# Kernel optimization log

Measured on AMD Instinct MI355X. Metric: run time of the kernel, lower is better.

Reference implementation:

```python
import jax, jax.numpy as jnp
import numpy as np

B, S, D, H = 2, 2048, 1024, 16
DEPTH = D // H


def setup_inputs() -> dict:
    key = jax.random.key(0)
    ks = jax.random.split(key, 10)
    std = 1.0 / np.sqrt(D)
    v = jax.random.normal(ks[0], (B, S, D), jnp.float32)
    q = jax.random.normal(ks[1], (B, S, D), jnp.float32)
    k = jax.random.normal(ks[2], (B, S, D), jnp.float32)
    # padding mask: 1.0 at masked (padded) key positions, 0.0 elsewhere
    mask = (jax.random.uniform(ks[3], (B, 1, 1, S)) < 0.1).astype(jnp.float32)
    Wq = jax.random.normal(ks[4], (D, D), jnp.float32) * std
    bq = jnp.zeros((D,), jnp.float32)
    Wv = jax.random.normal(ks[5], (D, D), jnp.float32) * std
    bv = jnp.zeros((D,), jnp.float32)
    Wo = jax.random.normal(ks[6], (D, D), jnp.float32) * std
    bo = jnp.zeros((D,), jnp.float32)
    return {"v": v, "q": q, "k": k, "mask": mask,
            "Wq": Wq, "bq": bq, "Wv": Wv, "bv": bv, "Wo": Wo, "bo": bo}


def _split_heads(x):
    # (B, S, D) -> (B, H, S, depth)
    return x.reshape(B, S, H, DEPTH).transpose(0, 2, 1, 3)


def reference(v, q, k, mask, Wq, bq, Wv, bv, Wo, bo):
    # NOTE: faithful to source, keys are projected with the QUERY weights
    # (mixedK = self.wQuery(k) in the original code).
    Q = _split_heads(q @ Wq + bq)
    K = _split_heads(k @ Wq + bq)
    V = _split_heads(v @ Wv + bv)
    scale = 1.0 / jnp.sqrt(jnp.asarray(DEPTH, jnp.float32))
    logits = jnp.einsum('bhqd,bhkd->bhqk', Q, K) * scale
    logits = logits + mask * (-1e9)
    attn = jax.nn.softmax(logits, axis=-1)
    out = jnp.einsum('bhqk,bhkd->bhqd', attn, V)
    out = out.transpose(0, 2, 1, 3).reshape(B, S, D)
    return out @ Wo + bo
```

## Files before the change

### kernel.cpp

```cpp
#include <hip/hip_runtime.h>
#include <cstddef>


namespace {

constexpr int Ss = 2048;
constexpr int Dd = 1024;
constexpr int Mm = 4096;
constexpr int NT = Ss / 64;
constexpr float QSCALE = 0.18033688f;

typedef unsigned short u16;
typedef __attribute__((ext_vector_type(8))) __bf16 bf16x8;
typedef __attribute__((ext_vector_type(4))) float f32x4;
typedef __attribute__((ext_vector_type(16))) float f32x16;
typedef __attribute__((ext_vector_type(4))) unsigned int u32x4;
typedef __attribute__((ext_vector_type(2))) unsigned int u32x2;
typedef __attribute__((ext_vector_type(8))) unsigned short us8;

__device__ __forceinline__ u16 bfc(float f) {
  __bf16 h = (__bf16)f;
  return __builtin_bit_cast(u16, h);
}
__device__ __forceinline__ unsigned pack2(float lo, float hi) {
  return (unsigned)bfc(lo) | ((unsigned)bfc(hi) << 16);
}

__device__ __forceinline__ void gload_lds16(const void* g, void* l) {
  __builtin_amdgcn_global_load_lds(
      (__attribute__((address_space(1))) void*)g,
      (__attribute__((address_space(3))) void*)l, 16, 0, 0);
}

__device__ __forceinline__ f32x4 mfma16(bf16x8 a, bf16x8 b, f32x4 c) {
  return __builtin_amdgcn_mfma_f32_16x16x32_bf16(a, b, c, 0, 0, 0);
}
__device__ __forceinline__ f32x16 mfma32(bf16x8 a, bf16x8 b, f32x16 c) {
  return __builtin_amdgcn_mfma_f32_32x32x16_bf16(a, b, c, 0, 0, 0);
}
__device__ __forceinline__ float exp2_fast(float x) {
  return __builtin_amdgcn_exp2f(x);
}

__device__ __forceinline__ void pl32swap(unsigned& a, unsigned& b) {
#if __has_builtin(__builtin_amdgcn_permlane32_swap)
  u32x2 r = __builtin_amdgcn_permlane32_swap(a, b, false, false);
  a = r[0];
  b = r[1];
#else
  unsigned ax = (unsigned)__shfl_xor((int)a, 32);
  unsigned bx = (unsigned)__shfl_xor((int)b, 32);
  bool hi = (threadIdx.x & 63) >= 32;
  unsigned na = hi ? bx : a;
  unsigned nb = hi ? b : ax;
  a = na;
  b = nb;
#endif
}

#define PIPE_BARRIER_V(N)                                  \
  do {                                                     \
    asm volatile("s_waitcnt vmcnt(" #N ")" ::: "memory");  \
    __builtin_amdgcn_sched_barrier(0);                     \
    __builtin_amdgcn_s_barrier();                          \
    __builtin_amdgcn_sched_barrier(0);                     \
  } while (0)

__device__ __forceinline__ int swz(int row, int col) {
  return row * 64 + ((((col >> 3) ^ (row & 7)) << 3) | (col & 7));
}
__device__ __forceinline__ int src_col(int lane) {
  return ((lane & 7) ^ (lane >> 3)) * 8;
}

__global__ __launch_bounds__(256) void wt_transpose(const float* __restrict__ W0,
                                                    const float* __restrict__ W1,
                                                    const float* __restrict__ W2,
                                                    u16* __restrict__ wsbase) {
  const float* W = (blockIdx.z == 0) ? W0 : (blockIdx.z == 1) ? W1 : W2;
  u16* WT = wsbase + (size_t)blockIdx.z * (1024 * 1024);
  __shared__ float tile[32][33];
  const int tid = threadIdx.x;
  const int tx = tid & 31;
  const int ty = tid >> 5;
  const int n0 = blockIdx.x * 32;
  const int k0 = blockIdx.y * 32;
#pragma unroll
  for (int i = 0; i < 4; ++i)
    tile[ty + i * 8][tx] = W[(size_t)(k0 + ty + i * 8) * 1024 + n0 + tx];
  __syncthreads();
  const int r = tid >> 3;
  const int c4 = (tid & 7) * 4;
  ushort4 o4 = make_ushort4(bfc(tile[c4 + 0][r]), bfc(tile[c4 + 1][r]),
                            bfc(tile[c4 + 2][r]), bfc(tile[c4 + 3][r]));
  *(ushort4*)(&WT[(size_t)(n0 + r) * 1024 + k0 + c4]) = o4;
}

__global__ __launch_bounds__(256) void cvt_bf16(const float* __restrict__ q,
                                                const float* __restrict__ k,
                                                const float* __restrict__ v,
                                                u16* __restrict__ qb,
                                                u16* __restrict__ kb,
                                                u16* __restrict__ vb) {
  const int which = (int)(blockIdx.x >> 11);
  const int blk = (int)(blockIdx.x & 2047);
  const float* src = (which == 0) ? q : (which == 1) ? k : v;
  u16* dst = (which == 0) ? qb : (which == 1) ? kb : vb;
  const int base = (blk * 256 + (int)threadIdx.x) * 8;
  const float4 a = *(const float4*)(src + base);
  const float4 b = *(const float4*)(src + base + 4);
  us8 o;
  o[0] = bfc(a.x); o[1] = bfc(a.y); o[2] = bfc(a.z); o[3] = bfc(a.w);
  o[4] = bfc(b.x); o[5] = bfc(b.y); o[6] = bfc(b.z); o[7] = bfc(b.w);
  *(us8*)(dst + base) = o;
}

__global__ __launch_bounds__(256) void proj_qkv(
    const u16* __restrict__ qb, const u16* __restrict__ kb,
    const u16* __restrict__ vb, const u16* __restrict__ WqT,
    const u16* __restrict__ WvT, const float* __restrict__ bq,
    const float* __restrict__ bv, const float* __restrict__ maskf,
    u16* __restrict__ Qp, u16* __restrict__ Kp, u16* __restrict__ VpT) {
  constexpr int K = 1024, N = 1024, M = 4096;
  __shared__ u16 As[128 * 64];
  __shared__ u16 Bs[128 * 64];
  const int lin = (int)blockIdx.x;
  const int xcd = lin & 7;
  const int j = lin >> 3;
  const int panel = xcd * 12 + (j >> 3);
  const int ntile = j & 7;
  const int z = panel >> 5;
  const int mtile = panel & 31;
  const int n0 = ntile * 128;
  const int m0 = mtile * 128;

  const u16* A = (z == 0) ? qb : (z == 1) ? kb : vb;
  const u16* Bt = (z == 2) ? WvT : WqT;
  const float* bias = (z == 2) ? bv : bq;
  const float cscale = (z == 0) ? QSCALE : 1.0f;

  const int tid = threadIdx.x;
  const int wid = tid >> 6;
  const int lane = tid & 63;
  const int g = lane >> 4;
  const int lr = lane & 15;
  const int wr = wid >> 1, wc = wid & 1;

  const f32x4 zero = {0.f, 0.f, 0.f, 0.f};
  f32x4 acc[4][4];
#pragma unroll
  for (int m = 0; m < 4; ++m)
#pragma unroll
    for (int n = 0; n < 4; ++n) acc[m][n] = zero;

  for (int kt = 0; kt < 16; ++kt) {
#pragma unroll
    for (int jj = 0; jj < 4; ++jj) {
      int rb = (wid * 4 + jj) * 8;
      gload_lds16(&A[(size_t)(m0 + rb + (lane >> 3)) * K + kt * 64 + src_col(lane)],
                  &As[rb * 64]);
      gload_lds16(&Bt[(size_t)(n0 + rb + (lane >> 3)) * K + kt * 64 + src_col(lane)],
                  &Bs[rb * 64]);
    }
    __syncthreads();
#pragma unroll
    for (int kk = 0; kk < 2; ++kk) {
      bf16x8 a[4], b[4];
#pragma unroll
      for (int m = 0; m < 4; ++m)
        a[m] = *(const bf16x8*)(&As[swz(wr * 64 + m * 16 + lr, kk * 32 + g * 8)]);
#pragma unroll
      for (int n = 0; n < 4; ++n)
        b[n] = *(const bf16x8*)(&Bs[swz(wc * 64 + n * 16 + lr, kk * 32 + g * 8)]);
#pragma unroll
      for (int m = 0; m < 4; ++m)
#pragma unroll
        for (int n = 0; n < 4; ++n) acc[m][n] = mfma16(a[m], b[n], acc[m][n]);
    }
    __syncthreads();
  }

#pragma unroll
  for (int n = 0; n < 4; ++n) {
    const int col = n0 + wc * 64 + n * 16 + lr;
    const float bv_ = bias[col];
#pragma unroll
    for (int m = 0; m < 4; ++m) {
      const int rowb = m0 + wr * 64 + m * 16 + g * 4;
      if (z == 2) {
        const f32x4 mk = *(const f32x4*)(&maskf[rowb]);
        ushort4 o4;
        o4.x = (mk[0] != 0.f) ? (u16)0 : bfc(acc[m][n][0] + bv_);
        o4.y = (mk[1] != 0.f) ? (u16)0 : bfc(acc[m][n][1] + bv_);
        o4.z = (mk[2] != 0.f) ? (u16)0 : bfc(acc[m][n][2] + bv_);
        o4.w = (mk[3] != 0.f) ? (u16)0 : bfc(acc[m][n][3] + bv_);
        *(ushort4*)(&VpT[(size_t)col * M + rowb]) = o4;
      } else {
        u16* Cp = (z == 0) ? Qp : Kp;
#pragma unroll
        for (int r = 0; r < 4; ++r)
          Cp[(size_t)(rowb + r) * N + col] = bfc((acc[m][n][r] + bv_) * cscale);
      }
    }
  }
}

__global__ __launch_bounds__(256) void gemm_o(const u16* __restrict__ Ap,
                                              const u16* __restrict__ Bt,
                                              const float* __restrict__ bias,
                                              float* __restrict__ Cp) {
  constexpr int K = 1024, N = 1024;
  __shared__ u16 As[3][128 * 64];
  __shared__ u16 Bs[3][64 * 64];
  const int lin = (int)blockIdx.x;
  const int xcd = lin & 7;
  const int j = lin >> 3;
  const int mtile = xcd * 4 + (j >> 4);
  const int ntile = j & 15;
  const int n0 = ntile * 64;
  const int m0 = mtile * 128;

  const int tid = threadIdx.x;
  const int wid = tid >> 6;
  const int lane = tid & 63;
  const int g = lane >> 4;
  const int lr = lane & 15;

  const f32x4 zero = {0.f, 0.f, 0.f, 0.f};
  f32x4 acc[2][4];
#pragma unroll
  for (int m = 0; m < 2; ++m)
#pragma unroll
    for (int n = 0; n < 4; ++n) acc[m][n] = zero;

  auto stage = [&](int kt, u16* as, u16* bs) {
#pragma unroll
    for (int jj = 0; jj < 4; ++jj) {
      int rb = (wid * 4 + jj) * 8;
      gload_lds16(&Ap[(size_t)(m0 + rb + (lane >> 3)) * K + kt * 64 + src_col(lane)],
                  as + rb * 64);
    }
#pragma unroll
    for (int jj = 0; jj < 2; ++jj) {
      int rb = (wid * 2 + jj) * 8;
      gload_lds16(&Bt[(size_t)(n0 + rb + (lane >> 3)) * K + kt * 64 + src_col(lane)],
                  bs + rb * 64);
    }
  };

  stage(0, As[0], Bs[0]);
  stage(1, As[1], Bs[1]);

  int b0 = 0;
  for (int kt = 0; kt < 16; ++kt) {
    if (kt < 15) PIPE_BARRIER_V(6);
    else         PIPE_BARRIER_V(0);
    if (kt + 2 < 16) {
      int b2 = b0 + 2; if (b2 >= 3) b2 -= 3;
      stage(kt + 2, As[b2], Bs[b2]);
    }
    const u16* as = As[b0];
    const u16* bs = Bs[b0];
#pragma unroll
    for (int kk = 0; kk < 2; ++kk) {
      bf16x8 a[2], b[4];
#pragma unroll
      for (int m = 0; m < 2; ++m)
        a[m] = *(const bf16x8*)(&as[swz(wid * 32 + m * 16 + lr, kk * 32 + g * 8)]);
#pragma unroll
      for (int n = 0; n < 4; ++n)
        b[n] = *(const bf16x8*)(&bs[swz(n * 16 + lr, kk * 32 + g * 8)]);
#pragma unroll
      for (int m = 0; m < 2; ++m)
#pragma unroll
        for (int n = 0; n < 4; ++n) acc[m][n] = mfma16(a[m], b[n], acc[m][n]);
    }
    b0 = (b0 == 2) ? 0 : b0 + 1;
  }
#pragma unroll
  for (int n = 0; n < 4; ++n) {
    const int col = n0 + n * 16 + lr;
    const float bv_ = bias[col];
#pragma unroll
    for (int m = 0; m < 2; ++m) {
      const int rowb = m0 + wid * 32 + m * 16 + g * 4;
#pragma unroll
      for (int r = 0; r < 4; ++r)
        Cp[(size_t)(rowb + r) * N + col] = acc[m][n][r] + bv_;
    }
  }
}

__global__ __launch_bounds__(512) void attn32(const u16* __restrict__ Qp,
                                              const u16* __restrict__ Kp,
                                              const u16* __restrict__ VpT,
                                              const float* __restrict__ mask,
                                              u16* __restrict__ Op) {
  __shared__ u16 smem[6 * 64 * 64];
  __shared__ u16 validall[Ss];
  const int tid = threadIdx.x;
  const int wid = tid >> 6;
  const int lane = tid & 63;
  const int l31 = lane & 31;
  const int hi = lane >> 5;
  const int qq = wid & 3;
  const int kh = wid >> 2;
  const int lin = (int)(blockIdx.x + (blockIdx.y << 4));
  const int wl = (lin & 7) * 64 + (lin >> 3);
  const int qt = wl & 15;
  const int bh = wl >> 4;
  const int b = bh >> 4;
  const int h = bh & 15;
  const int q0 = qt * 128;
  const size_t base = ((size_t)b * Ss) * Dd + (size_t)h * 64;
  const size_t vbase = (size_t)h * 64 * Mm + (size_t)b * Ss;
  const int qrow = q0 + qq * 32 + l31;

  auto stageKV = [&](int t, int buf) {
    const int key0 = t * 64;
    const int rb = wid * 8;
    gload_lds16(&Kp[base + (size_t)(key0 + rb + (lane >> 3)) * Dd + src_col(lane)],
                smem + buf * 4096 + rb * 64);
    gload_lds16(&VpT[vbase + (size_t)(rb + (lane >> 3)) * Mm + key0 + src_col(lane)],
                smem + (3 + buf) * 4096 + rb * 64);
  };

  float4 mk0, mk1;
  if (tid < 256) {
    mk0 = *(const float4*)(&mask[(size_t)b * Ss + tid * 8]);
    mk1 = *(const float4*)(&mask[(size_t)b * Ss + tid * 8 + 4]);
  }
  bf16x8 qf[4];
#pragma unroll
  for (int ks = 0; ks < 4; ++ks)
    qf[ks] = *(const bf16x8*)(&Qp[base + (size_t)qrow * Dd + ks * 16 + hi * 8]);

  stageKV(0, 0);
  stageKV(1, 1);

  if (tid < 256) {
    us8 vv;
    vv[0] = (mk0.x != 0.f) ? (u16)0 : (u16)0x3F80;
    vv[1] = (mk0.y != 0.f) ? (u16)0 : (u16)0x3F80;
    vv[2] = (mk0.z != 0.f) ? (u16)0 : (u16)0x3F80;
    vv[3] = (mk0.w != 0.f) ? (u16)0 : (u16)0x3F80;
    vv[4] = (mk1.x != 0.f) ? (u16)0 : (u16)0x3F80;
    vv[5] = (mk1.y != 0.f) ? (u16)0 : (u16)0x3F80;
    vv[6] = (mk1.z != 0.f) ? (u16)0 : (u16)0x3F80;
    vv[7] = (mk1.w != 0.f) ? (u16)0 : (u16)0x3F80;
    *(us8*)(&validall[tid * 8]) = vv;
  }
  asm volatile("s_waitcnt lgkmcnt(0)" ::: "memory");
  __builtin_amdgcn_sched_barrier(0);
  __builtin_amdgcn_s_barrier();
  __builtin_amdgcn_sched_barrier(0);

  f32x16 oacc[2], lacc, zero16;
#pragma unroll
  for (int r = 0; r < 16; ++r) zero16[r] = 0.f;
#pragma unroll
  for (int i = 0; i < 2; ++i)
#pragma unroll
    for (int r = 0; r < 16; ++r) oacc[i][r] = 0.f;
#pragma unroll
  for (int r = 0; r < 16; ++r) lacc[r] = 0.f;

  int b0 = 0;
  for (int t = 0; t < NT; ++t) {
    if (t < NT - 1) PIPE_BARRIER_V(2);
    else            PIPE_BARRIER_V(0);
    if (t + 2 < NT) {
      int b2 = b0 + 2; if (b2 >= 3) b2 -= 3;
      stageKV(t + 2, b2);
    }
    const u16* ks = smem + b0 * 4096;
    const u16* vt = smem + (3 + b0) * 4096;

    f32x16 sacc;
    {
      bf16x8 kf = *(const bf16x8*)(&ks[swz(kh * 32 + l31, 0 * 16 + hi * 8)]);
      sacc = mfma32(kf, qf[0], zero16);
    }
    __builtin_amdgcn_s_setprio(1);
#pragma unroll
    for (int ks_ = 1; ks_ < 4; ++ks_) {
      bf16x8 kf = *(const bf16x8*)(&ks[swz(kh * 32 + l31, ks_ * 16 + hi * 8)]);
      sacc = mfma32(kf, qf[ks_], sacc);
    }
    __builtin_amdgcn_s_setprio(0);

#pragma unroll
    for (int r = 0; r < 16; ++r) sacc[r] = exp2_fast(sacc[r]);

    bf16x8 pa[2];
#pragma unroll
    for (int slot = 0; slot < 2; ++slot) {
      const int bse = slot * 8;
      unsigned A0 = pack2(sacc[bse + 0], sacc[bse + 1]);
      unsigned A1 = pack2(sacc[bse + 2], sacc[bse + 3]);
      unsigned B0 = pack2(sacc[bse + 4], sacc[bse + 5]);
      unsigned B1 = pack2(sacc[bse + 6], sacc[bse + 7]);
      pl32swap(A0, B0);
      pl32swap(A1, B1);
      u32x4 w = {A0, A1, B0, B1};
      pa[slot] = __builtin_bit_cast(bf16x8, w);
    }

    __builtin_amdgcn_s_setprio(1);
#pragma unroll
    for (int slot = 0; slot < 2; ++slot) {
      const int kbase = t * 64 + kh * 32 + slot * 16 + hi * 8;
      bf16x8 vd = *(const bf16x8*)(&validall[kbase]);
#pragma unroll
      for (int dsub = 0; dsub < 2; ++dsub) {
        bf16x8 vf = *(const bf16x8*)(
            &vt[swz(dsub * 32 + l31, kh * 32 + slot * 16 + hi * 8)]);
        oacc[dsub] = mfma32(pa[slot], vf, oacc[dsub]);
      }
      lacc = mfma32(pa[slot], vd, lacc);
    }
    __builtin_amdgcn_s_setprio(0);

    b0 = (b0 == 2) ? 0 : b0 + 1;
  }

  __syncthreads();
  float* rbuf = (float*)smem;
  if (kh == 1) {
    float* p = rbuf + qq * 3072 + lane;
#pragma unroll
    for (int r = 0; r < 16; ++r) p[r * 64] = oacc[0][r];
#pragma unroll
    for (int r = 0; r < 16; ++r) p[(16 + r) * 64] = oacc[1][r];
#pragma unroll
    for (int r = 0; r < 16; ++r) p[(32 + r) * 64] = lacc[r];
  }
  __syncthreads();
  if (kh == 0) {
    const float* p = rbuf + qq * 3072 + lane;
#pragma unroll
    for (int r = 0; r < 16; ++r) oacc[0][r] += p[r * 64];
#pragma unroll
    for (int r = 0; r < 16; ++r) oacc[1][r] += p[(16 + r) * 64];
#pragma unroll
    for (int r = 0; r < 16; ++r) lacc[r] += p[(32 + r) * 64];

    float rl[16];
#pragma unroll
    for (int r = 0; r < 16; ++r) rl[r] = __builtin_amdgcn_rcpf(lacc[r]);
#pragma unroll
    for (int dsub = 0; dsub < 2; ++dsub) {
      const int col = h * 64 + dsub * 32 + l31;
#pragma unroll
      for (int r = 0; r < 16; ++r) {
        const int row = q0 + qq * 32 + (r & 3) + 8 * (r >> 2) + 4 * hi;
        Op[((size_t)b * Ss + row) * Dd + col] = bfc(oacc[dsub][r] * rl[r]);
      }
    }
  }
}

}

extern "C" void kernel_launch(void* const* d_in, const int* in_sizes, int n_in,
                              void* d_out, int out_size, void* d_ws, size_t ws_size,
                              hipStream_t stream) {
  (void)in_sizes; (void)n_in; (void)out_size; (void)ws_size;
  const float* v = (const float*)d_in[0];
  const float* q = (const float*)d_in[1];
  const float* k = (const float*)d_in[2];
  const float* mask = (const float*)d_in[3];
  const float* Wq = (const float*)d_in[4];
  const float* bq = (const float*)d_in[5];
  const float* Wv = (const float*)d_in[6];
  const float* bv = (const float*)d_in[7];
  const float* Wo = (const float*)d_in[8];
  const float* bo = (const float*)d_in[9];
  float* out = (float*)d_out;

  constexpr size_t MEG = 1024 * 1024;
  u16* ws = (u16*)d_ws;
  u16* WqT = ws;
  u16* WvT = ws + 1 * MEG;
  u16* WoT = ws + 2 * MEG;
  u16* qb  = ws + 3 * MEG;
  u16* kb  = ws + 7 * MEG;
  u16* vb  = ws + 11 * MEG;
  u16* Qp  = ws + 15 * MEG;
  u16* Kp  = ws + 19 * MEG;
  u16* VpT = ws + 23 * MEG;
  u16* AO  = qb;

  wt_transpose<<<dim3(32, 32, 3), 256, 0, stream>>>(Wq, Wv, Wo, ws);
  cvt_bf16<<<dim3(6144), 256, 0, stream>>>(q, k, v, qb, kb, vb);
  proj_qkv<<<dim3(768), 256, 0, stream>>>(qb, kb, vb, WqT, WvT, bq, bv, mask,
                                          Qp, Kp, VpT);
  attn32<<<dim3(16, 32), 512, 0, stream>>>(Qp, Kp, VpT, mask, AO);
  gemm_o<<<dim3(512), 256, 0, stream>>>(AO, WoT, bo, out);
}
```

Before: 130.0 us.

## Split attention over two key halves and merge partials in a combine kernel

The attention kernel now splits the 2048 keys into two halves handled by separate blocks, which doubles the grid. Each block writes unnormalized bf16 partial outputs and fp32 row sums to workspace, and a new combine kernel adds the two halves and normalizes. The K/V staging also drops from triple to double buffering, which shrinks LDS so more blocks can be resident per CU. In exchange it adds a kernel launch, extra global traffic for the partials, a shallower load pipeline, and rounding of the partial outputs to bf16 before they are summed.

```diff
diff --git a/kernel.cpp b/kernel.cpp
--- a/kernel.cpp
+++ b/kernel.cpp
@@ -7,7 +7,6 @@
 constexpr int Ss = 2048;
 constexpr int Dd = 1024;
 constexpr int Mm = 4096;
-constexpr int NT = Ss / 64;
 constexpr float QSCALE = 0.18033688f;
 
 typedef unsigned short u16;
@@ -21,6 +20,9 @@
 __device__ __forceinline__ u16 bfc(float f) {
   __bf16 h = (__bf16)f;
   return __builtin_bit_cast(u16, h);
+}
+__device__ __forceinline__ float bf2f(u16 u) {
+  return __builtin_bit_cast(float, (unsigned)u << 16);
 }
 __device__ __forceinline__ unsigned pack2(float lo, float hi) {
   return (unsigned)bfc(lo) | ((unsigned)bfc(hi) << 16);
@@ -295,9 +297,10 @@
                                               const u16* __restrict__ Kp,
                                               const u16* __restrict__ VpT,
                                               const float* __restrict__ mask,
-                                              u16* __restrict__ Op) {
-  __shared__ u16 smem[6 * 64 * 64];
-  __shared__ u16 validall[Ss];
+                                              u16* __restrict__ Opart,
+                                              float* __restrict__ lpart) {
+  __shared__ u16 smem[4 * 64 * 64];
+  __shared__ u16 valid[1024];
   const int tid = threadIdx.x;
   const int wid = tid >> 6;
   const int lane = tid & 63;
@@ -305,40 +308,42 @@
   const int hi = lane >> 5;
   const int qq = wid & 3;
   const int kh = wid >> 2;
-  const int lin = (int)(blockIdx.x + (blockIdx.y << 4));
-  const int wl = (lin & 7) * 64 + (lin >> 3);
+  const int lin = (int)(blockIdx.x + (blockIdx.y << 5));
+  const int wl = (lin & 7) * 128 + (lin >> 3);
   const int qt = wl & 15;
-  const int bh = wl >> 4;
+  const int bhks = wl >> 4;
+  const int ks = bhks & 1;
+  const int bh = bhks >> 1;
   const int b = bh >> 4;
   const int h = bh & 15;
   const int q0 = qt * 128;
   const size_t base = ((size_t)b * Ss) * Dd + (size_t)h * 64;
   const size_t vbase = (size_t)h * 64 * Mm + (size_t)b * Ss;
   const int qrow = q0 + qq * 32 + l31;
+  const int pidx = (bh * 16 + qt) * 2 + ks;
 
   auto stageKV = [&](int t, int buf) {
-    const int key0 = t * 64;
+    const int key0 = ks * 1024 + t * 64;
     const int rb = wid * 8;
     gload_lds16(&Kp[base + (size_t)(key0 + rb + (lane >> 3)) * Dd + src_col(lane)],
                 smem + buf * 4096 + rb * 64);
     gload_lds16(&VpT[vbase + (size_t)(rb + (lane >> 3)) * Mm + key0 + src_col(lane)],
-                smem + (3 + buf) * 4096 + rb * 64);
+                smem + (2 + buf) * 4096 + rb * 64);
   };
 
   float4 mk0, mk1;
-  if (tid < 256) {
-    mk0 = *(const float4*)(&mask[(size_t)b * Ss + tid * 8]);
-    mk1 = *(const float4*)(&mask[(size_t)b * Ss + tid * 8 + 4]);
+  if (tid < 128) {
+    mk0 = *(const float4*)(&mask[(size_t)b * Ss + ks * 1024 + tid * 8]);
+    mk1 = *(const float4*)(&mask[(size_t)b * Ss + ks * 1024 + tid * 8 + 4]);
   }
   bf16x8 qf[4];
 #pragma unroll
-  for (int ks = 0; ks < 4; ++ks)
-    qf[ks] = *(const bf16x8*)(&Qp[base + (size_t)qrow * Dd + ks * 16 + hi * 8]);
+  for (int d = 0; d < 4; ++d)
+    qf[d] = *(const bf16x8*)(&Qp[base + (size_t)qrow * Dd + d * 16 + hi * 8]);
 
   stageKV(0, 0);
-  stageKV(1, 1);
-
-  if (tid < 256) {
+
+  if (tid < 128) {
     us8 vv;
     vv[0] = (mk0.x != 0.f) ? (u16)0 : (u16)0x3F80;
     vv[1] = (mk0.y != 0.f) ? (u16)0 : (u16)0x3F80;
@@ -348,7 +353,7 @@
     vv[5] = (mk1.y != 0.f) ? (u16)0 : (u16)0x3F80;
     vv[6] = (mk1.z != 0.f) ? (u16)0 : (u16)0x3F80;
     vv[7] = (mk1.w != 0.f) ? (u16)0 : (u16)0x3F80;
-    *(us8*)(&validall[tid * 8]) = vv;
+    *(us8*)(&valid[tid * 8]) = vv;
   }
   asm volatile("s_waitcnt lgkmcnt(0)" ::: "memory");
   __builtin_amdgcn_sched_barrier(0);
@@ -365,27 +370,22 @@
 #pragma unroll
   for (int r = 0; r < 16; ++r) lacc[r] = 0.f;
 
-  int b0 = 0;
-  for (int t = 0; t < NT; ++t) {
-    if (t < NT - 1) PIPE_BARRIER_V(2);
-    else            PIPE_BARRIER_V(0);
-    if (t + 2 < NT) {
-      int b2 = b0 + 2; if (b2 >= 3) b2 -= 3;
-      stageKV(t + 2, b2);
-    }
-    const u16* ks = smem + b0 * 4096;
-    const u16* vt = smem + (3 + b0) * 4096;
+  for (int t = 0; t < 16; ++t) {
+    PIPE_BARRIER_V(0);
+    if (t + 1 < 16) stageKV(t + 1, (t + 1) & 1);
+    const u16* ksb = smem + (t & 1) * 4096;
+    const u16* vtb = smem + (2 + (t & 1)) * 4096;
 
     f32x16 sacc;
     {
-      bf16x8 kf = *(const bf16x8*)(&ks[swz(kh * 32 + l31, 0 * 16 + hi * 8)]);
+      bf16x8 kf = *(const bf16x8*)(&ksb[swz(kh * 32 + l31, 0 * 16 + hi * 8)]);
       sacc = mfma32(kf, qf[0], zero16);
     }
     __builtin_amdgcn_s_setprio(1);
 #pragma unroll
-    for (int ks_ = 1; ks_ < 4; ++ks_) {
-      bf16x8 kf = *(const bf16x8*)(&ks[swz(kh * 32 + l31, ks_ * 16 + hi * 8)]);
-      sacc = mfma32(kf, qf[ks_], sacc);
+    for (int d = 1; d < 4; ++d) {
+      bf16x8 kf = *(const bf16x8*)(&ksb[swz(kh * 32 + l31, d * 16 + hi * 8)]);
+      sacc = mfma32(kf, qf[d], sacc);
     }
     __builtin_amdgcn_s_setprio(0);
 
@@ -410,54 +410,81 @@
 #pragma unroll
     for (int slot = 0; slot < 2; ++slot) {
       const int kbase = t * 64 + kh * 32 + slot * 16 + hi * 8;
-      bf16x8 vd = *(const bf16x8*)(&validall[kbase]);
+      bf16x8 vd = *(const bf16x8*)(&valid[kbase]);
 #pragma unroll
       for (int dsub = 0; dsub < 2; ++dsub) {
         bf16x8 vf = *(const bf16x8*)(
-            &vt[swz(dsub * 32 + l31, kh * 32 + slot * 16 + hi * 8)]);
+            &vtb[swz(dsub * 32 + l31, kh * 32 + slot * 16 + hi * 8)]);
         oacc[dsub] = mfma32(pa[slot], vf, oacc[dsub]);
       }
       lacc = mfma32(pa[slot], vd, lacc);
     }
     __builtin_amdgcn_s_setprio(0);
-
-    b0 = (b0 == 2) ? 0 : b0 + 1;
-  }
-
-  __syncthreads();
+  }
+
   float* rbuf = (float*)smem;
-  if (kh == 1) {
-    float* p = rbuf + qq * 3072 + lane;
-#pragma unroll
-    for (int r = 0; r < 16; ++r) p[r * 64] = oacc[0][r];
-#pragma unroll
-    for (int r = 0; r < 16; ++r) p[(16 + r) * 64] = oacc[1][r];
-#pragma unroll
-    for (int r = 0; r < 16; ++r) p[(32 + r) * 64] = lacc[r];
-  }
-  __syncthreads();
-  if (kh == 0) {
-    const float* p = rbuf + qq * 3072 + lane;
-#pragma unroll
-    for (int r = 0; r < 16; ++r) oacc[0][r] += p[r * 64];
-#pragma unroll
-    for (int r = 0; r < 16; ++r) oacc[1][r] += p[(16 + r) * 64];
-#pragma unroll
-    for (int r = 0; r < 16; ++r) lacc[r] += p[(32 + r) * 64];
-
-    float rl[16];
-#pragma unroll
-    for (int r = 0; r < 16; ++r) rl[r] = __builtin_amdgcn_rcpf(lacc[r]);
-#pragma unroll
-    for (int dsub = 0; dsub < 2; ++dsub) {
-      const int col = h * 64 + dsub * 32 + l31;
-#pragma unroll
-      for (int r = 0; r < 16; ++r) {
-        const int row = q0 + qq * 32 + (r & 3) + 8 * (r >> 2) + 4 * hi;
-        Op[((size_t)b * Ss + row) * Dd + col] = bfc(oacc[dsub][r] * rl[r]);
+  for (int round = 0; round < 2; ++round) {
+    __syncthreads();
+    if ((qq >> 1) == round && kh == 1) {
+      float* p = rbuf + (qq & 1) * 3072 + lane;
+#pragma unroll
+      for (int r = 0; r < 16; ++r) p[r * 64] = oacc[0][r];
+#pragma unroll
+      for (int r = 0; r < 16; ++r) p[(16 + r) * 64] = oacc[1][r];
+#pragma unroll
+      for (int r = 0; r < 16; ++r) p[(32 + r) * 64] = lacc[r];
+    }
+    __syncthreads();
+    if ((qq >> 1) == round && kh == 0) {
+      const float* p = rbuf + (qq & 1) * 3072 + lane;
+#pragma unroll
+      for (int r = 0; r < 16; ++r) oacc[0][r] += p[r * 64];
+#pragma unroll
+      for (int r = 0; r < 16; ++r) oacc[1][r] += p[(16 + r) * 64];
+#pragma unroll
+      for (int r = 0; r < 16; ++r) lacc[r] += p[(32 + r) * 64];
+
+      u16* ob = Opart + (size_t)pidx * 8192;
+#pragma unroll
+      for (int dsub = 0; dsub < 2; ++dsub)
+#pragma unroll
+        for (int r = 0; r < 16; ++r) {
+          const int rl = qq * 32 + (r & 3) + 8 * (r >> 2) + 4 * hi;
+          ob[rl * 64 + dsub * 32 + l31] = bfc(oacc[dsub][r]);
+        }
+      if (l31 == 0) {
+#pragma unroll
+        for (int r = 0; r < 16; ++r) {
+          const int rl = qq * 32 + (r & 3) + 8 * (r >> 2) + 4 * hi;
+          lpart[(size_t)pidx * 128 + rl] = lacc[r];
+        }
       }
     }
   }
+}
+
+__global__ __launch_bounds__(256) void combine(const u16* __restrict__ Opart,
+                                               const float* __restrict__ lpart,
+                                               u16* __restrict__ AO) {
+  const int e = (int)blockIdx.x * 256 + (int)threadIdx.x;
+  const int d8 = e & 7;
+  const int h = (e >> 3) & 15;
+  const int row = e >> 7;
+  const int b = row >> 11;
+  const int srow = row & 2047;
+  const int qt = srow >> 7;
+  const int r = srow & 127;
+  const int pbase = ((b * 16 + h) * 16 + qt) * 2;
+  const size_t off = (size_t)r * 64 + d8 * 8;
+
+  const us8 o0 = *(const us8*)(&Opart[(size_t)pbase * 8192 + off]);
+  const us8 o1 = *(const us8*)(&Opart[(size_t)(pbase + 1) * 8192 + off]);
+  const float l = lpart[(size_t)pbase * 128 + r] + lpart[(size_t)(pbase + 1) * 128 + r];
+  const float rl = __builtin_amdgcn_rcpf(l);
+  us8 o;
+#pragma unroll
+  for (int j = 0; j < 8; ++j) o[j] = bfc((bf2f(o0[j]) + bf2f(o1[j])) * rl);
+  *(us8*)(&AO[(size_t)row * 1024 + h * 64 + d8 * 8]) = o;
 }
 
 }
@@ -490,11 +517,14 @@
   u16* Kp  = ws + 19 * MEG;
   u16* VpT = ws + 23 * MEG;
   u16* AO  = qb;
+  u16* Opart = kb;
+  float* lpart = (float*)WqT;
 
   wt_transpose<<<dim3(32, 32, 3), 256, 0, stream>>>(Wq, Wv, Wo, ws);
   cvt_bf16<<<dim3(6144), 256, 0, stream>>>(q, k, v, qb, kb, vb);
   proj_qkv<<<dim3(768), 256, 0, stream>>>(qb, kb, vb, WqT, WvT, bq, bv, mask,
                                           Qp, Kp, VpT);
-  attn32<<<dim3(16, 32), 512, 0, stream>>>(Qp, Kp, VpT, mask, AO);
+  attn32<<<dim3(32, 32), 512, 0, stream>>>(Qp, Kp, VpT, mask, Opart, lpart);
+  combine<<<dim3(2048), 256, 0, stream>>>(Opart, lpart, AO);
   gemm_o<<<dim3(512), 256, 0, stream>>>(AO, WoT, bo, out);
 }
```

Measured after the change: 138.8 us. +6.8%, slower.

## Restructure attention tiles to 128 keys with 2x4 wave split and additive mask

Applied to the files above, without the earlier changes.

The attention kernel now stages 128-key K/V tiles with double buffering instead of 64-key triple buffering. The eight waves are split as 2 query groups by 4 key groups, and each wave handles 64 query rows so every K fragment load feeds two MFMA chains. The padding mask becomes an additive bias preloaded into the score accumulator, and the row sums are computed with shuffles rather than an extra MFMA against a validity vector. The cost is a four-way cross-wave reduction of outputs and sums at the end, done in several synchronised passes, plus more registers per wave, which may reduce occupancy.

```diff
diff --git a/kernel.cpp b/kernel.cpp
--- a/kernel.cpp
+++ b/kernel.cpp
@@ -7,8 +7,8 @@
 constexpr int Ss = 2048;
 constexpr int Dd = 1024;
 constexpr int Mm = 4096;
-constexpr int NT = Ss / 64;
 constexpr float QSCALE = 0.18033688f;
+constexpr float NEG2 = -1.442695041e9f;
 
 typedef unsigned short u16;
 typedef __attribute__((ext_vector_type(8))) __bf16 bf16x8;
@@ -61,6 +61,13 @@
 #define PIPE_BARRIER_V(N)                                  \
   do {                                                     \
     asm volatile("s_waitcnt vmcnt(" #N ")" ::: "memory");  \
+    __builtin_amdgcn_sched_barrier(0);                     \
+    __builtin_amdgcn_s_barrier();                          \
+    __builtin_amdgcn_sched_barrier(0);                     \
+  } while (0)
+
+#define PLAIN_BARRIER()                                    \
+  do {                                                     \
     __builtin_amdgcn_sched_barrier(0);                     \
     __builtin_amdgcn_s_barrier();                          \
     __builtin_amdgcn_sched_barrier(0);                     \
@@ -296,15 +303,16 @@
                                               const u16* __restrict__ VpT,
                                               const float* __restrict__ mask,
                                               u16* __restrict__ Op) {
-  __shared__ u16 smem[6 * 64 * 64];
-  __shared__ u16 validall[Ss];
+  __shared__ u16 Ks[2][128 * 64];
+  __shared__ u16 Vt[2][2][64 * 64];
+  __shared__ float msall[2048];
   const int tid = threadIdx.x;
   const int wid = tid >> 6;
   const int lane = tid & 63;
   const int l31 = lane & 31;
   const int hi = lane >> 5;
-  const int qq = wid & 3;
-  const int kh = wid >> 2;
+  const int qq = wid & 1;
+  const int kh = wid >> 1;
   const int lin = (int)(blockIdx.x + (blockIdx.y << 4));
   const int wl = (lin & 7) * 64 + (lin >> 3);
   const int qt = wl & 15;
@@ -314,149 +322,195 @@
   const int q0 = qt * 128;
   const size_t base = ((size_t)b * Ss) * Dd + (size_t)h * 64;
   const size_t vbase = (size_t)h * 64 * Mm + (size_t)b * Ss;
-  const int qrow = q0 + qq * 32 + l31;
 
   auto stageKV = [&](int t, int buf) {
-    const int key0 = t * 64;
-    const int rb = wid * 8;
-    gload_lds16(&Kp[base + (size_t)(key0 + rb + (lane >> 3)) * Dd + src_col(lane)],
-                smem + buf * 4096 + rb * 64);
-    gload_lds16(&VpT[vbase + (size_t)(rb + (lane >> 3)) * Mm + key0 + src_col(lane)],
-                smem + (3 + buf) * 4096 + rb * 64);
+    const int key0 = t * 128;
+#pragma unroll
+    for (int j = 0; j < 2; ++j) {
+      const int rb = wid * 16 + j * 8;
+      gload_lds16(&Kp[base + (size_t)(key0 + rb + (lane >> 3)) * Dd + src_col(lane)],
+                  &Ks[buf][rb * 64]);
+    }
+#pragma unroll
+    for (int kc = 0; kc < 2; ++kc) {
+      const int rb = wid * 8;
+      gload_lds16(&VpT[vbase + (size_t)(rb + (lane >> 3)) * Mm + key0 + kc * 64 + src_col(lane)],
+                  &Vt[buf][kc][rb * 64]);
+    }
   };
 
-  float4 mk0, mk1;
-  if (tid < 256) {
-    mk0 = *(const float4*)(&mask[(size_t)b * Ss + tid * 8]);
-    mk1 = *(const float4*)(&mask[(size_t)b * Ss + tid * 8 + 4]);
-  }
-  bf16x8 qf[4];
-#pragma unroll
-  for (int ks = 0; ks < 4; ++ks)
-    qf[ks] = *(const bf16x8*)(&Qp[base + (size_t)qrow * Dd + ks * 16 + hi * 8]);
+  bf16x8 qf[2][4];
+#pragma unroll
+  for (int qs = 0; qs < 2; ++qs) {
+    const int qrow = q0 + qq * 64 + qs * 32 + l31;
+#pragma unroll
+    for (int d = 0; d < 4; ++d)
+      qf[qs][d] = *(const bf16x8*)(&Qp[base + (size_t)qrow * Dd + d * 16 + hi * 8]);
+  }
+  const float4 mk = *(const float4*)(&mask[(size_t)b * Ss + tid * 4]);
 
   stageKV(0, 0);
   stageKV(1, 1);
 
-  if (tid < 256) {
-    us8 vv;
-    vv[0] = (mk0.x != 0.f) ? (u16)0 : (u16)0x3F80;
-    vv[1] = (mk0.y != 0.f) ? (u16)0 : (u16)0x3F80;
-    vv[2] = (mk0.z != 0.f) ? (u16)0 : (u16)0x3F80;
-    vv[3] = (mk0.w != 0.f) ? (u16)0 : (u16)0x3F80;
-    vv[4] = (mk1.x != 0.f) ? (u16)0 : (u16)0x3F80;
-    vv[5] = (mk1.y != 0.f) ? (u16)0 : (u16)0x3F80;
-    vv[6] = (mk1.z != 0.f) ? (u16)0 : (u16)0x3F80;
-    vv[7] = (mk1.w != 0.f) ? (u16)0 : (u16)0x3F80;
-    *(us8*)(&validall[tid * 8]) = vv;
+  {
+    f32x4 s = {mk.x * NEG2, mk.y * NEG2, mk.z * NEG2, mk.w * NEG2};
+    *(f32x4*)(&msall[tid * 4]) = s;
   }
   asm volatile("s_waitcnt lgkmcnt(0)" ::: "memory");
-  __builtin_amdgcn_sched_barrier(0);
-  __builtin_amdgcn_s_barrier();
-  __builtin_amdgcn_sched_barrier(0);
-
-  f32x16 oacc[2], lacc, zero16;
-#pragma unroll
-  for (int r = 0; r < 16; ++r) zero16[r] = 0.f;
-#pragma unroll
-  for (int i = 0; i < 2; ++i)
-#pragma unroll
-    for (int r = 0; r < 16; ++r) oacc[i][r] = 0.f;
-#pragma unroll
-  for (int r = 0; r < 16; ++r) lacc[r] = 0.f;
-
-  int b0 = 0;
-  for (int t = 0; t < NT; ++t) {
-    if (t < NT - 1) PIPE_BARRIER_V(2);
-    else            PIPE_BARRIER_V(0);
-    if (t + 2 < NT) {
-      int b2 = b0 + 2; if (b2 >= 3) b2 -= 3;
-      stageKV(t + 2, b2);
-    }
-    const u16* ks = smem + b0 * 4096;
-    const u16* vt = smem + (3 + b0) * 4096;
-
-    f32x16 sacc;
-    {
-      bf16x8 kf = *(const bf16x8*)(&ks[swz(kh * 32 + l31, 0 * 16 + hi * 8)]);
-      sacc = mfma32(kf, qf[0], zero16);
-    }
+  PLAIN_BARRIER();
+
+  f32x16 oacc[2][2];
+#pragma unroll
+  for (int qs = 0; qs < 2; ++qs)
+#pragma unroll
+    for (int ds = 0; ds < 2; ++ds)
+#pragma unroll
+      for (int r = 0; r < 16; ++r) oacc[qs][ds][r] = 0.f;
+  float lsum[2] = {0.f, 0.f};
+
+  for (int t = 0; t < 16; ++t) {
+    if (t < 15) PIPE_BARRIER_V(4);
+    else        PIPE_BARRIER_V(0);
+    const u16* ksb = Ks[t & 1];
+    const u16* vkc = &Vt[t & 1][kh >> 1][0];
+    const int koff = (kh & 1) * 32;
+    const float* msp = &msall[t * 128 + kh * 32];
+
+    bf16x8 kf[4];
+#pragma unroll
+    for (int d = 0; d < 4; ++d)
+      kf[d] = *(const bf16x8*)(&ksb[swz(kh * 32 + l31, d * 16 + hi * 8)]);
+
+    f32x4 mm[4];
+#pragma unroll
+    for (int a = 0; a < 4; ++a)
+      mm[a] = *(const f32x4*)(&msp[a * 8 + hi * 4]);
+    f32x16 sacc[2];
+#pragma unroll
+    for (int qs = 0; qs < 2; ++qs)
+#pragma unroll
+      for (int a = 0; a < 4; ++a)
+#pragma unroll
+        for (int jj = 0; jj < 4; ++jj) sacc[qs][a * 4 + jj] = mm[a][jj];
+
     __builtin_amdgcn_s_setprio(1);
 #pragma unroll
-    for (int ks_ = 1; ks_ < 4; ++ks_) {
-      bf16x8 kf = *(const bf16x8*)(&ks[swz(kh * 32 + l31, ks_ * 16 + hi * 8)]);
-      sacc = mfma32(kf, qf[ks_], sacc);
-    }
+    for (int qs = 0; qs < 2; ++qs)
+#pragma unroll
+      for (int d = 0; d < 4; ++d)
+        sacc[qs] = mfma32(kf[d], qf[qs][d], sacc[qs]);
     __builtin_amdgcn_s_setprio(0);
 
 #pragma unroll
-    for (int r = 0; r < 16; ++r) sacc[r] = exp2_fast(sacc[r]);
-
-    bf16x8 pa[2];
-#pragma unroll
-    for (int slot = 0; slot < 2; ++slot) {
-      const int bse = slot * 8;
-      unsigned A0 = pack2(sacc[bse + 0], sacc[bse + 1]);
-      unsigned A1 = pack2(sacc[bse + 2], sacc[bse + 3]);
-      unsigned B0 = pack2(sacc[bse + 4], sacc[bse + 5]);
-      unsigned B1 = pack2(sacc[bse + 6], sacc[bse + 7]);
-      pl32swap(A0, B0);
-      pl32swap(A1, B1);
-      u32x4 w = {A0, A1, B0, B1};
-      pa[slot] = __builtin_bit_cast(bf16x8, w);
-    }
-
+    for (int qs = 0; qs < 2; ++qs)
+#pragma unroll
+      for (int r = 0; r < 16; ++r) sacc[qs][r] = exp2_fast(sacc[qs][r]);
+
+#pragma unroll
+    for (int qs = 0; qs < 2; ++qs) {
+      float sm = sacc[qs][0];
+#pragma unroll
+      for (int r = 1; r < 16; ++r) sm += sacc[qs][r];
+      lsum[qs] += sm + __shfl_xor(sm, 32);
+    }
+
+    bf16x8 pa[2][2];
+#pragma unroll
+    for (int qs = 0; qs < 2; ++qs)
+#pragma unroll
+      for (int slot = 0; slot < 2; ++slot) {
+        const int bse = slot * 8;
+        unsigned A0 = pack2(sacc[qs][bse + 0], sacc[qs][bse + 1]);
+        unsigned A1 = pack2(sacc[qs][bse + 2], sacc[qs][bse + 3]);
+        unsigned B0 = pack2(sacc[qs][bse + 4], sacc[qs][bse + 5]);
+        unsigned B1 = pack2(sacc[qs][bse + 6], sacc[qs][bse + 7]);
+        pl32swap(A0, B0);
+        pl32swap(A1, B1);
+        u32x4 w = {A0, A1, B0, B1};
+        pa[qs][slot] = __builtin_bit_cast(bf16x8, w);
+      }
+
+    bf16x8 vfr[2][2];
+#pragma unroll
+    for (int ds = 0; ds < 2; ++ds)
+#pragma unroll
+      for (int slot = 0; slot < 2; ++slot)
+        vfr[ds][slot] = *(const bf16x8*)(
+            &vkc[swz(ds * 32 + l31, koff + slot * 16 + hi * 8)]);
     __builtin_amdgcn_s_setprio(1);
 #pragma unroll
-    for (int slot = 0; slot < 2; ++slot) {
-      const int kbase = t * 64 + kh * 32 + slot * 16 + hi * 8;
-      bf16x8 vd = *(const bf16x8*)(&validall[kbase]);
-#pragma unroll
-      for (int dsub = 0; dsub < 2; ++dsub) {
-        bf16x8 vf = *(const bf16x8*)(
-            &vt[swz(dsub * 32 + l31, kh * 32 + slot * 16 + hi * 8)]);
-        oacc[dsub] = mfma32(pa[slot], vf, oacc[dsub]);
+    for (int qs = 0; qs < 2; ++qs)
+#pragma unroll
+      for (int ds = 0; ds < 2; ++ds)
+#pragma unroll
+        for (int slot = 0; slot < 2; ++slot)
+          oacc[qs][ds] = mfma32(pa[qs][slot], vfr[ds][slot], oacc[qs][ds]);
+    __builtin_amdgcn_s_setprio(0);
+
+    PLAIN_BARRIER();
+    if (t + 2 < 16) stageKV(t + 2, t & 1);
+  }
+
+  PLAIN_BARRIER();
+  if (kh > 0) {
+#pragma unroll
+    for (int qs = 0; qs < 2; ++qs)
+      msall[qs * 192 + (kh - 1) * 64 + qq * 32 + l31] = lsum[qs];
+  }
+  __syncthreads();
+  f32x4 rlv[2];
+  if (kh == 0) {
+#pragma unroll
+    for (int qs = 0; qs < 2; ++qs) {
+      float lt = lsum[qs];
+#pragma unroll
+      for (int j = 0; j < 3; ++j)
+        lt += msall[qs * 192 + j * 64 + qq * 32 + l31];
+      msall[512 + qs * 64 + qq * 32 + l31] = __builtin_amdgcn_rcpf(lt);
+    }
+    asm volatile("s_waitcnt lgkmcnt(0)" ::: "memory");
+    __builtin_amdgcn_sched_barrier(0);
+  }
+  float* rbuf = (float*)&Ks[0][0];
+#pragma unroll
+  for (int qs = 0; qs < 2; ++qs)
+#pragma unroll
+    for (int ds = 0; ds < 2; ++ds) {
+      __syncthreads();
+      if (kh > 0) {
+        float* p = rbuf + ((kh - 1) * 2 + qq) * 1024 + lane;
+#pragma unroll
+        for (int r = 0; r < 16; ++r) p[r * 64] = oacc[qs][ds][r];
       }
-      lacc = mfma32(pa[slot], vd, lacc);
-    }
-    __builtin_amdgcn_s_setprio(0);
-
-    b0 = (b0 == 2) ? 0 : b0 + 1;
-  }
-
-  __syncthreads();
-  float* rbuf = (float*)smem;
-  if (kh == 1) {
-    float* p = rbuf + qq * 3072 + lane;
-#pragma unroll
-    for (int r = 0; r < 16; ++r) p[r * 64] = oacc[0][r];
-#pragma unroll
-    for (int r = 0; r < 16; ++r) p[(16 + r) * 64] = oacc[1][r];
-#pragma unroll
-    for (int r = 0; r < 16; ++r) p[(32 + r) * 64] = lacc[r];
-  }
-  __syncthreads();
+      __syncthreads();
+      if (kh == 0) {
+#pragma unroll
+        for (int j = 0; j < 3; ++j) {
+          const float* p = rbuf + (j * 2 + qq) * 1024 + lane;
+#pragma unroll
+          for (int r = 0; r < 16; ++r) oacc[qs][ds][r] += p[r * 64];
+        }
+      }
+    }
   if (kh == 0) {
-    const float* p = rbuf + qq * 3072 + lane;
-#pragma unroll
-    for (int r = 0; r < 16; ++r) oacc[0][r] += p[r * 64];
-#pragma unroll
-    for (int r = 0; r < 16; ++r) oacc[1][r] += p[(16 + r) * 64];
-#pragma unroll
-    for (int r = 0; r < 16; ++r) lacc[r] += p[(32 + r) * 64];
-
-    float rl[16];
-#pragma unroll
-    for (int r = 0; r < 16; ++r) rl[r] = __builtin_amdgcn_rcpf(lacc[r]);
-#pragma unroll
-    for (int dsub = 0; dsub < 2; ++dsub) {
-      const int col = h * 64 + dsub * 32 + l31;
-#pragma unroll
-      for (int r = 0; r < 16; ++r) {
-        const int row = q0 + qq * 32 + (r & 3) + 8 * (r >> 2) + 4 * hi;
-        Op[((size_t)b * Ss + row) * Dd + col] = bfc(oacc[dsub][r] * rl[r]);
+    f32x4 rl[2][4];
+#pragma unroll
+    for (int qs = 0; qs < 2; ++qs)
+#pragma unroll
+      for (int a = 0; a < 4; ++a)
+        rl[qs][a] = *(const f32x4*)(&msall[512 + qs * 64 + qq * 32 + a * 8 + hi * 4]);
+#pragma unroll
+    for (int qs = 0; qs < 2; ++qs)
+#pragma unroll
+      for (int ds = 0; ds < 2; ++ds) {
+        const int col = h * 64 + ds * 32 + l31;
+#pragma unroll
+        for (int r = 0; r < 16; ++r) {
+          const int row = q0 + qq * 64 + qs * 32 + (r & 3) + 8 * (r >> 2) + 4 * hi;
+          Op[((size_t)b * Ss + row) * Dd + col] =
+              bfc(oacc[qs][ds][r] * rl[qs][r >> 2][r & 3]);
+        }
       }
-    }
   }
 }
 
```

Result: slower. 145.5 us (+11.9%).

## Merge prep kernels and restructure attention loop with additive mask and 4-buffer staging

Applied to the files above, without the earlier changes.

Fuses the weight transpose and bf16 conversion into one prep launch to remove a kernel launch. In the attention kernel, the mask is now added to the logits by seeding the QK accumulator with a scaled mask bias, replacing the extra MFMA that computed the row sum against a validity vector. The row sum is instead formed by in-register adds plus a lane shuffle. The K/V pipeline goes from a triple buffer to four buffers loaded two tiles at a time, with one barrier per pair of tiles. This uses more LDS and may expose more load latency, because each barrier waits for all outstanding loads (vmcnt 0).

```diff
diff --git a/kernel.cpp b/kernel.cpp
--- a/kernel.cpp
+++ b/kernel.cpp
@@ -7,8 +7,8 @@
 constexpr int Ss = 2048;
 constexpr int Dd = 1024;
 constexpr int Mm = 4096;
-constexpr int NT = Ss / 64;
 constexpr float QSCALE = 0.18033688f;
+constexpr float NEG2 = -1.442695041e9f;
 
 typedef unsigned short u16;
 typedef __attribute__((ext_vector_type(8))) __bf16 bf16x8;
@@ -73,46 +73,51 @@
   return ((lane & 7) ^ (lane >> 3)) * 8;
 }
 
-__global__ __launch_bounds__(256) void wt_transpose(const float* __restrict__ W0,
-                                                    const float* __restrict__ W1,
-                                                    const float* __restrict__ W2,
-                                                    u16* __restrict__ wsbase) {
-  const float* W = (blockIdx.z == 0) ? W0 : (blockIdx.z == 1) ? W1 : W2;
-  u16* WT = wsbase + (size_t)blockIdx.z * (1024 * 1024);
+__global__ __launch_bounds__(256) void prep(const float* __restrict__ W0,
+                                            const float* __restrict__ W1,
+                                            const float* __restrict__ W2,
+                                            const float* __restrict__ q,
+                                            const float* __restrict__ k,
+                                            const float* __restrict__ v,
+                                            u16* __restrict__ wsbase,
+                                            u16* __restrict__ qb,
+                                            u16* __restrict__ kb,
+                                            u16* __restrict__ vb) {
   __shared__ float tile[32][33];
+  const int blk = (int)blockIdx.x;
   const int tid = threadIdx.x;
-  const int tx = tid & 31;
-  const int ty = tid >> 5;
-  const int n0 = blockIdx.x * 32;
-  const int k0 = blockIdx.y * 32;
-#pragma unroll
-  for (int i = 0; i < 4; ++i)
-    tile[ty + i * 8][tx] = W[(size_t)(k0 + ty + i * 8) * 1024 + n0 + tx];
-  __syncthreads();
-  const int r = tid >> 3;
-  const int c4 = (tid & 7) * 4;
-  ushort4 o4 = make_ushort4(bfc(tile[c4 + 0][r]), bfc(tile[c4 + 1][r]),
-                            bfc(tile[c4 + 2][r]), bfc(tile[c4 + 3][r]));
-  *(ushort4*)(&WT[(size_t)(n0 + r) * 1024 + k0 + c4]) = o4;
-}
-
-__global__ __launch_bounds__(256) void cvt_bf16(const float* __restrict__ q,
-                                                const float* __restrict__ k,
-                                                const float* __restrict__ v,
-                                                u16* __restrict__ qb,
-                                                u16* __restrict__ kb,
-                                                u16* __restrict__ vb) {
-  const int which = (int)(blockIdx.x >> 11);
-  const int blk = (int)(blockIdx.x & 2047);
-  const float* src = (which == 0) ? q : (which == 1) ? k : v;
-  u16* dst = (which == 0) ? qb : (which == 1) ? kb : vb;
-  const int base = (blk * 256 + (int)threadIdx.x) * 8;
-  const float4 a = *(const float4*)(src + base);
-  const float4 b = *(const float4*)(src + base + 4);
-  us8 o;
-  o[0] = bfc(a.x); o[1] = bfc(a.y); o[2] = bfc(a.z); o[3] = bfc(a.w);
-  o[4] = bfc(b.x); o[5] = bfc(b.y); o[6] = bfc(b.z); o[7] = bfc(b.w);
-  *(us8*)(dst + base) = o;
+  if (blk < 3072) {
+    const int z = blk >> 10;
+    const int rem = blk & 1023;
+    const int n0 = (rem & 31) * 32;
+    const int k0 = (rem >> 5) * 32;
+    const float* W = (z == 0) ? W0 : (z == 1) ? W1 : W2;
+    u16* WT = wsbase + (size_t)z * (1024 * 1024);
+    const int tx = tid & 31;
+    const int ty = tid >> 5;
+#pragma unroll
+    for (int i = 0; i < 4; ++i)
+      tile[ty + i * 8][tx] = W[(size_t)(k0 + ty + i * 8) * 1024 + n0 + tx];
+    __syncthreads();
+    const int r = tid >> 3;
+    const int c4 = (tid & 7) * 4;
+    ushort4 o4 = make_ushort4(bfc(tile[c4 + 0][r]), bfc(tile[c4 + 1][r]),
+                              bfc(tile[c4 + 2][r]), bfc(tile[c4 + 3][r]));
+    *(ushort4*)(&WT[(size_t)(n0 + r) * 1024 + k0 + c4]) = o4;
+  } else {
+    const int e = blk - 3072;
+    const int which = e >> 11;
+    const int b2 = e & 2047;
+    const float* src = (which == 0) ? q : (which == 1) ? k : v;
+    u16* dst = (which == 0) ? qb : (which == 1) ? kb : vb;
+    const int base = (b2 * 256 + tid) * 8;
+    const float4 a = *(const float4*)(src + base);
+    const float4 b = *(const float4*)(src + base + 4);
+    us8 o;
+    o[0] = bfc(a.x); o[1] = bfc(a.y); o[2] = bfc(a.z); o[3] = bfc(a.w);
+    o[4] = bfc(b.x); o[5] = bfc(b.y); o[6] = bfc(b.z); o[7] = bfc(b.w);
+    *(us8*)(dst + base) = o;
+  }
 }
 
 __global__ __launch_bounds__(256) void proj_qkv(
@@ -296,8 +301,8 @@
                                               const u16* __restrict__ VpT,
                                               const float* __restrict__ mask,
                                               u16* __restrict__ Op) {
-  __shared__ u16 smem[6 * 64 * 64];
-  __shared__ u16 validall[Ss];
+  __shared__ u16 smem[8 * 64 * 64];
+  __shared__ float msall[Ss];
   const int tid = threadIdx.x;
   const int wid = tid >> 6;
   const int lane = tid & 63;
@@ -322,106 +327,102 @@
     gload_lds16(&Kp[base + (size_t)(key0 + rb + (lane >> 3)) * Dd + src_col(lane)],
                 smem + buf * 4096 + rb * 64);
     gload_lds16(&VpT[vbase + (size_t)(rb + (lane >> 3)) * Mm + key0 + src_col(lane)],
-                smem + (3 + buf) * 4096 + rb * 64);
+                smem + (4 + buf) * 4096 + rb * 64);
   };
 
-  float4 mk0, mk1;
-  if (tid < 256) {
-    mk0 = *(const float4*)(&mask[(size_t)b * Ss + tid * 8]);
-    mk1 = *(const float4*)(&mask[(size_t)b * Ss + tid * 8 + 4]);
-  }
+  const float4 mk = *(const float4*)(&mask[(size_t)b * Ss + tid * 4]);
   bf16x8 qf[4];
 #pragma unroll
-  for (int ks = 0; ks < 4; ++ks)
-    qf[ks] = *(const bf16x8*)(&Qp[base + (size_t)qrow * Dd + ks * 16 + hi * 8]);
+  for (int d = 0; d < 4; ++d)
+    qf[d] = *(const bf16x8*)(&Qp[base + (size_t)qrow * Dd + d * 16 + hi * 8]);
 
   stageKV(0, 0);
   stageKV(1, 1);
 
-  if (tid < 256) {
-    us8 vv;
-    vv[0] = (mk0.x != 0.f) ? (u16)0 : (u16)0x3F80;
-    vv[1] = (mk0.y != 0.f) ? (u16)0 : (u16)0x3F80;
-    vv[2] = (mk0.z != 0.f) ? (u16)0 : (u16)0x3F80;
-    vv[3] = (mk0.w != 0.f) ? (u16)0 : (u16)0x3F80;
-    vv[4] = (mk1.x != 0.f) ? (u16)0 : (u16)0x3F80;
-    vv[5] = (mk1.y != 0.f) ? (u16)0 : (u16)0x3F80;
-    vv[6] = (mk1.z != 0.f) ? (u16)0 : (u16)0x3F80;
-    vv[7] = (mk1.w != 0.f) ? (u16)0 : (u16)0x3F80;
-    *(us8*)(&validall[tid * 8]) = vv;
+  {
+    f32x4 s = {mk.x * NEG2, mk.y * NEG2, mk.z * NEG2, mk.w * NEG2};
+    *(f32x4*)(&msall[tid * 4]) = s;
   }
   asm volatile("s_waitcnt lgkmcnt(0)" ::: "memory");
   __builtin_amdgcn_sched_barrier(0);
   __builtin_amdgcn_s_barrier();
   __builtin_amdgcn_sched_barrier(0);
 
-  f32x16 oacc[2], lacc, zero16;
-#pragma unroll
-  for (int r = 0; r < 16; ++r) zero16[r] = 0.f;
+  f32x16 oacc[2];
 #pragma unroll
   for (int i = 0; i < 2; ++i)
 #pragma unroll
     for (int r = 0; r < 16; ++r) oacc[i][r] = 0.f;
-#pragma unroll
-  for (int r = 0; r < 16; ++r) lacc[r] = 0.f;
-
-  int b0 = 0;
-  for (int t = 0; t < NT; ++t) {
-    if (t < NT - 1) PIPE_BARRIER_V(2);
-    else            PIPE_BARRIER_V(0);
-    if (t + 2 < NT) {
-      int b2 = b0 + 2; if (b2 >= 3) b2 -= 3;
-      stageKV(t + 2, b2);
-    }
-    const u16* ks = smem + b0 * 4096;
-    const u16* vt = smem + (3 + b0) * 4096;
-
-    f32x16 sacc;
-    {
-      bf16x8 kf = *(const bf16x8*)(&ks[swz(kh * 32 + l31, 0 * 16 + hi * 8)]);
-      sacc = mfma32(kf, qf[0], zero16);
-    }
-    __builtin_amdgcn_s_setprio(1);
-#pragma unroll
-    for (int ks_ = 1; ks_ < 4; ++ks_) {
-      bf16x8 kf = *(const bf16x8*)(&ks[swz(kh * 32 + l31, ks_ * 16 + hi * 8)]);
-      sacc = mfma32(kf, qf[ks_], sacc);
-    }
-    __builtin_amdgcn_s_setprio(0);
-
-#pragma unroll
-    for (int r = 0; r < 16; ++r) sacc[r] = exp2_fast(sacc[r]);
-
-    bf16x8 pa[2];
-#pragma unroll
-    for (int slot = 0; slot < 2; ++slot) {
-      const int bse = slot * 8;
-      unsigned A0 = pack2(sacc[bse + 0], sacc[bse + 1]);
-      unsigned A1 = pack2(sacc[bse + 2], sacc[bse + 3]);
-      unsigned B0 = pack2(sacc[bse + 4], sacc[bse + 5]);
-      unsigned B1 = pack2(sacc[bse + 6], sacc[bse + 7]);
-      pl32swap(A0, B0);
-      pl32swap(A1, B1);
-      u32x4 w = {A0, A1, B0, B1};
-      pa[slot] = __builtin_bit_cast(bf16x8, w);
-    }
-
-    __builtin_amdgcn_s_setprio(1);
-#pragma unroll
-    for (int slot = 0; slot < 2; ++slot) {
-      const int kbase = t * 64 + kh * 32 + slot * 16 + hi * 8;
-      bf16x8 vd = *(const bf16x8*)(&validall[kbase]);
-#pragma unroll
-      for (int dsub = 0; dsub < 2; ++dsub) {
-        bf16x8 vf = *(const bf16x8*)(
-            &vt[swz(dsub * 32 + l31, kh * 32 + slot * 16 + hi * 8)]);
-        oacc[dsub] = mfma32(pa[slot], vf, oacc[dsub]);
+  float lsum = 0.f;
+
+  for (int i = 0; i < 16; ++i) {
+    PIPE_BARRIER_V(0);
+    if (i < 15) {
+      stageKV(2 * i + 2, (2 * i + 2) & 3);
+      stageKV(2 * i + 3, (2 * i + 3) & 3);
+    }
+#pragma unroll
+    for (int u = 0; u < 2; ++u) {
+      const int t = 2 * i + u;
+      const int buf = t & 3;
+      const u16* ks = smem + buf * 4096;
+      const u16* vt = smem + (4 + buf) * 4096;
+      const float* msp = &msall[t * 64 + kh * 32];
+
+      f32x16 sacc;
+#pragma unroll
+      for (int a = 0; a < 4; ++a) {
+        const f32x4 mv = *(const f32x4*)(&msp[a * 8 + hi * 4]);
+#pragma unroll
+        for (int jj = 0; jj < 4; ++jj) sacc[a * 4 + jj] = mv[jj];
       }
-      lacc = mfma32(pa[slot], vd, lacc);
-    }
-    __builtin_amdgcn_s_setprio(0);
-
-    b0 = (b0 == 2) ? 0 : b0 + 1;
+      __builtin_amdgcn_s_setprio(1);
+#pragma unroll
+      for (int d = 0; d < 4; ++d) {
+        bf16x8 kf = *(const bf16x8*)(&ks[swz(kh * 32 + l31, d * 16 + hi * 8)]);
+        sacc = mfma32(kf, qf[d], sacc);
+      }
+      __builtin_amdgcn_s_setprio(0);
+
+#pragma unroll
+      for (int r = 0; r < 16; ++r) sacc[r] = exp2_fast(sacc[r]);
+
+      {
+        float sm[8];
+#pragma unroll
+        for (int r = 0; r < 8; ++r) sm[r] = sacc[r] + sacc[r + 8];
+#pragma unroll
+        for (int s = 4; s >= 1; s >>= 1)
+#pragma unroll
+          for (int r = 0; r < s; ++r) sm[r] += sm[r + s];
+        lsum += sm[0] + __shfl_xor(sm[0], 32);
+      }
+
+      bf16x8 pa[2];
+#pragma unroll
+      for (int slot = 0; slot < 2; ++slot) {
+        const int bse = slot * 8;
+        unsigned A0 = pack2(sacc[bse + 0], sacc[bse + 1]);
+        unsigned A1 = pack2(sacc[bse + 2], sacc[bse + 3]);
+        unsigned B0 = pack2(sacc[bse + 4], sacc[bse + 5]);
+        unsigned B1 = pack2(sacc[bse + 6], sacc[bse + 7]);
+        pl32swap(A0, B0);
+        pl32swap(A1, B1);
+        u32x4 w = {A0, A1, B0, B1};
+        pa[slot] = __builtin_bit_cast(bf16x8, w);
+      }
+
+      __builtin_amdgcn_s_setprio(1);
+#pragma unroll
+      for (int slot = 0; slot < 2; ++slot)
+#pragma unroll
+        for (int dsub = 0; dsub < 2; ++dsub) {
+          bf16x8 vf = *(const bf16x8*)(
+              &vt[swz(dsub * 32 + l31, kh * 32 + slot * 16 + hi * 8)]);
+          oacc[dsub] = mfma32(pa[slot], vf, oacc[dsub]);
+        }
+      __builtin_amdgcn_s_setprio(0);
+    }
   }
 
   __syncthreads();
@@ -432,8 +433,7 @@
     for (int r = 0; r < 16; ++r) p[r * 64] = oacc[0][r];
 #pragma unroll
     for (int r = 0; r < 16; ++r) p[(16 + r) * 64] = oacc[1][r];
-#pragma unroll
-    for (int r = 0; r < 16; ++r) p[(32 + r) * 64] = lacc[r];
+    if (hi == 0) rbuf[12288 + qq * 32 + l31] = lsum;
   }
   __syncthreads();
   if (kh == 0) {
@@ -442,19 +442,21 @@
     for (int r = 0; r < 16; ++r) oacc[0][r] += p[r * 64];
 #pragma unroll
     for (int r = 0; r < 16; ++r) oacc[1][r] += p[(16 + r) * 64];
-#pragma unroll
-    for (int r = 0; r < 16; ++r) lacc[r] += p[(32 + r) * 64];
-
-    float rl[16];
-#pragma unroll
-    for (int r = 0; r < 16; ++r) rl[r] = __builtin_amdgcn_rcpf(lacc[r]);
+    const float ltot = lsum + rbuf[12288 + qq * 32 + l31];
+    float* lrow = rbuf + 12800 + qq * 32;
+    if (hi == 0) lrow[l31] = __builtin_amdgcn_rcpf(ltot);
+    f32x4 rl[4];
+#pragma unroll
+    for (int a = 0; a < 4; ++a)
+      rl[a] = *(const f32x4*)(&lrow[a * 8 + hi * 4]);
 #pragma unroll
     for (int dsub = 0; dsub < 2; ++dsub) {
       const int col = h * 64 + dsub * 32 + l31;
 #pragma unroll
       for (int r = 0; r < 16; ++r) {
         const int row = q0 + qq * 32 + (r & 3) + 8 * (r >> 2) + 4 * hi;
-        Op[((size_t)b * Ss + row) * Dd + col] = bfc(oacc[dsub][r] * rl[r]);
+        Op[((size_t)b * Ss + row) * Dd + col] =
+            bfc(oacc[dsub][r] * rl[r >> 2][r & 3]);
       }
     }
   }
@@ -491,8 +493,7 @@
   u16* VpT = ws + 23 * MEG;
   u16* AO  = qb;
 
-  wt_transpose<<<dim3(32, 32, 3), 256, 0, stream>>>(Wq, Wv, Wo, ws);
-  cvt_bf16<<<dim3(6144), 256, 0, stream>>>(q, k, v, qb, kb, vb);
+  prep<<<dim3(3072 + 6144), 256, 0, stream>>>(Wq, Wv, Wo, q, k, v, ws, qb, kb, vb);
   proj_qkv<<<dim3(768), 256, 0, stream>>>(qb, kb, vb, WqT, WvT, bq, bv, mask,
                                           Qp, Kp, VpT);
   attn32<<<dim3(16, 32), 512, 0, stream>>>(Qp, Kp, VpT, mask, AO);
```

Measured after the change: 127.4 us (median of 2 runs). 1.02x faster.
